# Kernel tuning notes

Hardware: AMD Instinct MI355X
Metric: run time of the kernel (lower is better)

## Reference

```python
import jax, jax.numpy as jnp
import numpy as np

EPS = 1e-5
HEADS = 2


def _batch_norm(x, gamma, beta, axes):
    # Training-mode batch norm (biased variance), channel axis = 1.
    m = jnp.mean(x, axes, keepdims=True)
    v = jnp.mean((x - m) ** 2, axes, keepdims=True)
    shape = [1] * x.ndim
    shape[1] = x.shape[1]
    return (x - m) * jax.lax.rsqrt(v + EPS) * gamma.reshape(shape) + beta.reshape(shape)


def setup_inputs() -> dict:
    key = jax.random.key(0)
    ks = jax.random.split(key, 6)
    b, n, H, W = 64, 2, 32, 32
    dim = H * W            # 1024
    inner = dim * HEADS    # 2048
    s = 0.02
    return {
        "x": jax.random.normal(ks[0], (b, n, H, W), jnp.float32),
        "Wq": jax.random.normal(ks[1], (inner, dim), jnp.float32) * s,
        "Wk": jax.random.normal(ks[2], (inner, dim), jnp.float32) * s,
        "Wv": jax.random.normal(ks[3], (inner, dim), jnp.float32) * s,
        "Wo": jax.random.normal(ks[4], (dim, inner), jnp.float32) * s,
        "bo": jnp.zeros((dim,), jnp.float32),
        "g_q": jnp.ones((2,), jnp.float32), "b_q": jnp.zeros((2,), jnp.float32),
        "g_k": jnp.ones((2,), jnp.float32), "b_k": jnp.zeros((2,), jnp.float32),
        "g_v": jnp.ones((2,), jnp.float32), "b_v": jnp.zeros((2,), jnp.float32),
        "g_bn": jnp.ones((2,), jnp.float32), "b_bn": jnp.zeros((2,), jnp.float32),
    }


def reference(x, Wq, Wk, Wv, Wo, bo, g_q, b_q, g_k, b_k, g_v, b_v, g_bn, b_bn):
    b, n, H, W = x.shape
    h = HEADS
    dim = H * W
    xf = x.reshape(b, n, dim)

    # to_q/to_k/to_v: Linear (no bias) + BatchNorm1d over channel dim n=2
    q = _batch_norm(xf @ Wq.T, g_q, b_q, (0, 2))  # (b, n, h*dim)
    k = _batch_norm(xf @ Wk.T, g_k, b_k, (0, 2))
    v = _batch_norm(xf @ Wv.T, g_v, b_v, (0, 2))

    def split_heads(t):  # b n (h d) -> b h n d
        return t.reshape(b, n, h, dim).transpose(0, 2, 1, 3)

    q, k, v = split_heads(q), split_heads(k), split_heads(v)

    # linear (kernelized) attention
    k_cumsum = k.sum(axis=-2)                                   # (b, h, d)
    D_inv = 1.0 / jnp.einsum('bhnd,bhd->bhn', q, k_cumsum)      # (b, h, n)
    context = jnp.einsum('bhnd,bhne->bhde', k, v)               # (b, h, d, d)
    out = jnp.einsum('bhde,bhnd,bhn->bhne', context, q, D_inv)  # (b, h, n, d)

    out = out.transpose(0, 2, 1, 3).reshape(b, n, h * dim)      # b h n d -> b n (h d)
    out = out @ Wo.T + bo                                       # to_out
    out = out.reshape(b, n, H, W)                               # dropout p=0 is identity
    return _batch_norm(out, g_bn, b_bn, (0, 2, 3))              # BatchNorm2d(2)
```

## Files before the change

kernel.cpp:

```cpp
#include <hip/hip_runtime.h>
#include <stdint.h>

typedef __bf16 bf16x8 __attribute__((ext_vector_type(8)));
typedef float f32x4 __attribute__((ext_vector_type(4)));

#define EPS 1e-5f

#define OFF_SQ    0
#define OFF_Q     4096
#define OFF_AHI   (OFF_Q + 3145728)
#define OFF_SO    (OFF_AHI + 524288)
#define OFF_PROJ  (OFF_SO + 4096)

static __device__ __forceinline__ unsigned short f2b(float f) {
  return __builtin_bit_cast(unsigned short, (__bf16)f);
}

__device__ __forceinline__ float wave_red(float v) {
#pragma unroll
  for (int o = 32; o > 0; o >>= 1) v += __shfl_down(v, o);
  return v;
}

#define GLDS16(g, l)                                             \
  __builtin_amdgcn_global_load_lds(                              \
      (const __attribute__((address_space(1))) void*)(g),        \
      (__attribute__((address_space(3))) void*)(l), 16, 0, 0)

static __device__ __forceinline__ void frag_split(const float* base, int p0,
                                                  bf16x8& hi, bf16x8& lo) {
  float4 v0 = *(const float4*)(base + p0 * 4);
  float4 v1 = *(const float4*)(base + p0 * 4 + 4);
  float a[8] = {v0.x, v0.y, v0.z, v0.w, v1.x, v1.y, v1.z, v1.w};
#pragma unroll
  for (int i = 0; i < 8; ++i) {
    __bf16 h = (__bf16)a[i];
    hi[i] = h;
    lo[i] = (__bf16)(a[i] - (float)h);
  }
}
static __device__ __forceinline__ bf16x8 frag_cvt(const float* base, int p0) {
  float4 v0 = *(const float4*)(base + p0 * 4);
  float4 v1 = *(const float4*)(base + p0 * 4 + 4);
  bf16x8 r;
  r[0] = (__bf16)v0.x; r[1] = (__bf16)v0.y; r[2] = (__bf16)v0.z; r[3] = (__bf16)v0.w;
  r[4] = (__bf16)v1.x; r[5] = (__bf16)v1.y; r[6] = (__bf16)v1.z; r[7] = (__bf16)v1.w;
  return r;
}

__global__ __launch_bounds__(256) void qkv_gemm(const float* __restrict__ x,
                                                const float* __restrict__ Wq,
                                                const float* __restrict__ Wk,
                                                const float* __restrict__ Wv,
                                                float* __restrict__ qkv,
                                                float* __restrict__ sq) {
  __shared__ alignas(16) float Af[3][128 * 64];
  __shared__ alignas(16) float Bf[3][32 * 64];
  __shared__ float red[16];

  int mat = blockIdx.x >> 6;
  int nt  = blockIdx.x & 63;
  const float* W = (mat == 0) ? Wq : ((mat == 1) ? Wk : Wv);
  float* outp = qkv + mat * 262144;

  int tid = threadIdx.x, w = tid >> 6, lane = tid & 63;
  int rsel = lane >> 4, ch = lane & 15;

#define STAGE_Q(c, tt) do {                                                      \
    _Pragma("unroll")                                                            \
    for (int j = 0; j < 8; ++j) {                                                \
      int rl = w * 32 + j * 4 + rsel;                                            \
      GLDS16(x + rl * 1024 + (tt) * 64 + ((ch ^ ((rl & 7) << 1)) << 2),          \
             &Af[c][(w * 32 + j * 4) * 64]);                                     \
    }                                                                            \
    _Pragma("unroll")                                                            \
    for (int j = 0; j < 2; ++j) {                                                \
      int rl = w * 8 + j * 4 + rsel;                                             \
      GLDS16(W + (nt * 32 + rl) * 1024 + (tt) * 64 +                             \
                 ((ch ^ ((rl & 7) << 1)) << 2),                                  \
             &Bf[c][(w * 8 + j * 4) * 64]);                                      \
    }                                                                            \
  } while (0)

  f32x4 acc[2][2];
#pragma unroll
  for (int m = 0; m < 2; ++m)
#pragma unroll
    for (int n = 0; n < 2; ++n) acc[m][n] = (f32x4){0.f, 0.f, 0.f, 0.f};

  STAGE_Q(0, 0);
  STAGE_Q(1, 1);
  __syncthreads();

#pragma unroll
  for (int t = 0; t < 16; ++t) {
    const int c = t % 3;
    bf16x8 fah[2][2], fal[2][2], fbh[2][2], fbl[2][2];
#pragma unroll
    for (int ks = 0; ks < 2; ++ks) {
      int kc = ks * 4 + rsel;
#pragma unroll
      for (int m = 0; m < 2; ++m) {
        int ra = w * 32 + m * 16 + (lane & 15);
        int p0 = (kc * 2) ^ ((ra & 7) << 1);
        frag_split(&Af[c][ra * 64], p0, fah[ks][m], fal[ks][m]);
      }
#pragma unroll
      for (int n = 0; n < 2; ++n) {
        int rb = n * 16 + (lane & 15);
        int p0 = (kc * 2) ^ ((rb & 7) << 1);
        frag_split(&Bf[c][rb * 64], p0, fbh[ks][n], fbl[ks][n]);
      }
    }
    if (t < 14) { STAGE_Q((t + 2) % 3, t + 2); }
#pragma unroll
    for (int ks = 0; ks < 2; ++ks)
#pragma unroll
      for (int m = 0; m < 2; ++m)
#pragma unroll
        for (int n = 0; n < 2; ++n) {
          acc[m][n] = __builtin_amdgcn_mfma_f32_16x16x32_bf16(fah[ks][m], fbh[ks][n], acc[m][n], 0, 0, 0);
          acc[m][n] = __builtin_amdgcn_mfma_f32_16x16x32_bf16(fah[ks][m], fbl[ks][n], acc[m][n], 0, 0, 0);
          acc[m][n] = __builtin_amdgcn_mfma_f32_16x16x32_bf16(fal[ks][m], fbh[ks][n], acc[m][n], 0, 0, 0);
        }
    if (t < 15) {
      if (t < 14) { asm volatile("s_waitcnt vmcnt(10) lgkmcnt(0)" ::: "memory"); }
      else        { asm volatile("s_waitcnt vmcnt(0) lgkmcnt(0)" ::: "memory"); }
      __builtin_amdgcn_sched_barrier(0);
      __builtin_amdgcn_s_barrier();
      __builtin_amdgcn_sched_barrier(0);
    }
  }
#undef STAGE_Q

  float s0 = 0, q0 = 0, s1 = 0, q1 = 0;
#pragma unroll
  for (int m = 0; m < 2; ++m)
#pragma unroll
    for (int n = 0; n < 2; ++n)
#pragma unroll
      for (int r = 0; r < 4; ++r) {
        int row = w * 32 + m * 16 + (lane >> 4) * 4 + r;
        int col = nt * 32 + n * 16 + (lane & 15);
        float v = acc[m][n][r];
        outp[row * 2048 + col] = v;
        if (r & 1) { s1 += v; q1 += v * v; } else { s0 += v; q0 += v * v; }
      }
  s0 = wave_red(s0); q0 = wave_red(q0); s1 = wave_red(s1); q1 = wave_red(q1);
  if (lane == 0) { red[w * 4 + 0] = s0; red[w * 4 + 1] = q0; red[w * 4 + 2] = s1; red[w * 4 + 3] = q1; }
  __syncthreads();
  if (tid == 0) {
    float a0 = 0, a1 = 0, a2 = 0, a3 = 0;
    for (int i = 0; i < 4; ++i) { a0 += red[i * 4 + 0]; a1 += red[i * 4 + 1]; a2 += red[i * 4 + 2]; a3 += red[i * 4 + 3]; }
    *(float4*)(sq + blockIdx.x * 4) = (float4){a0, a1, a2, a3};
  }
}

__global__ __launch_bounds__(256) void attn_kernel(const float* __restrict__ qkv,
                                                   const float* __restrict__ sq,
                                                   ushort* __restrict__ ahi,
                                                   const float* __restrict__ g_q, const float* __restrict__ b_q,
                                                   const float* __restrict__ g_k, const float* __restrict__ b_k,
                                                   const float* __restrict__ g_v, const float* __restrict__ b_v) {
  __shared__ float sm[12];
  __shared__ float red[16];
  __shared__ float bc[4];
  int bh = blockIdx.x, b = bh >> 1, h = bh & 1;
  int tid = threadIdx.x, w = tid >> 6, lane = tid & 63;

  if (tid < 192) {
    float4 p = *(const float4*)(sq + tid * 4);
    float a0 = wave_red(p.x), a1 = wave_red(p.y), a2 = wave_red(p.z), a3 = wave_red(p.w);
    if (lane == 0) { sm[w * 4 + 0] = a0; sm[w * 4 + 1] = a1; sm[w * 4 + 2] = a2; sm[w * 4 + 3] = a3; }
  }
  __syncthreads();

  const float cnt = 131072.f;
  float qs[2], qo[2], kc_[2], ko[2], vs[2], vo[2];
#pragma unroll
  for (int c = 0; c < 2; ++c) {
    float m, var, inv;
    m = sm[0 + 2 * c] / cnt; var = sm[1 + 2 * c] / cnt - m * m; inv = rsqrtf(var + EPS);
    qs[c] = g_q[c] * inv; qo[c] = b_q[c] - m * qs[c];
    m = sm[4 + 2 * c] / cnt; var = sm[5 + 2 * c] / cnt - m * m; inv = rsqrtf(var + EPS);
    kc_[c] = g_k[c] * inv; ko[c] = b_k[c] - m * kc_[c];
    m = sm[8 + 2 * c] / cnt; var = sm[9 + 2 * c] / cnt - m * m; inv = rsqrtf(var + EPS);
    vs[c] = g_v[c] * inv; vo[c] = b_v[c] - m * vs[c];
  }

  const float* Q = qkv;
  const float* K = qkv + 262144;
  const float* V = qkv + 524288;
  const float* q0p = Q + (b * 2 + 0) * 2048 + h * 1024;
  const float* q1p = Q + (b * 2 + 1) * 2048 + h * 1024;
  const float* k0p = K + (b * 2 + 0) * 2048 + h * 1024;
  const float* k1p = K + (b * 2 + 1) * 2048 + h * 1024;
  const float* v0p = V + (b * 2 + 0) * 2048 + h * 1024;
  const float* v1p = V + (b * 2 + 1) * 2048 + h * 1024;

  float p00 = 0, p01 = 0, p10 = 0, p11 = 0;
#pragma unroll
  for (int i = 0; i < 4; ++i) {
    int d = tid + i * 256;
    float a0 = q0p[d] * qs[0] + qo[0];
    float a1 = q1p[d] * qs[1] + qo[1];
    float c0 = k0p[d] * kc_[0] + ko[0];
    float c1 = k1p[d] * kc_[1] + ko[1];
    p00 += a0 * c0; p01 += a0 * c1; p10 += a1 * c0; p11 += a1 * c1;
  }
  p00 = wave_red(p00); p01 = wave_red(p01); p10 = wave_red(p10); p11 = wave_red(p11);
  if (lane == 0) { red[w * 4 + 0] = p00; red[w * 4 + 1] = p01; red[w * 4 + 2] = p10; red[w * 4 + 3] = p11; }
  __syncthreads();
  if (tid < 4) bc[tid] = red[0 + tid] + red[4 + tid] + red[8 + tid] + red[12 + tid];
  __syncthreads();
  float s00 = bc[0], s01 = bc[1], s10 = bc[2], s11 = bc[3];
  float di0 = 1.f / (s00 + s01), di1 = 1.f / (s10 + s11);
  int o0 = (b * 2 + 0) * 2048 + h * 1024;
  int o1 = (b * 2 + 1) * 2048 + h * 1024;
#pragma unroll
  for (int i = 0; i < 4; ++i) {
    int d = tid + i * 256;
    float v0 = v0p[d] * vs[0] + vo[0];
    float v1 = v1p[d] * vs[1] + vo[1];
    ahi[o0 + d] = f2b((s00 * v0 + s01 * v1) * di0);
    ahi[o1 + d] = f2b((s10 * v0 + s11 * v1) * di1);
  }
}

__global__ __launch_bounds__(256) void out_gemm(const ushort* __restrict__ ahi,
                                                const float* __restrict__ Wo,
                                                const float* __restrict__ bo,
                                                float* __restrict__ proj,
                                                float* __restrict__ so) {
  __shared__ alignas(16) ushort Ab[3][64 * 128];
  __shared__ alignas(16) float  Bf[3][16 * 128];
  __shared__ float red[16];

  int mt = blockIdx.x >> 6;
  int nt = blockIdx.x & 63;

  int tid = threadIdx.x, w = tid >> 6, lane = tid & 63;
  int rsel4 = lane >> 4, ch16 = lane & 15;
  int rsel2 = lane >> 5, ch32 = lane & 31;

#define STAGE_O(c, tt) do {                                                      \
    _Pragma("unroll")                                                            \
    for (int j = 0; j < 4; ++j) {                                                \
      int rl = w * 16 + j * 4 + rsel4;                                           \
      GLDS16(ahi + (mt * 64 + rl) * 2048 + (tt) * 128 +                          \
                 ((ch16 ^ (rl & 7)) << 3),                                       \
             &Ab[c][(w * 16 + j * 4) * 128]);                                    \
    }                                                                            \
    _Pragma("unroll")                                                            \
    for (int j = 0; j < 2; ++j) {                                                \
      int rl = w * 4 + j * 2 + rsel2;                                            \
      GLDS16(Wo + (nt * 16 + rl) * 2048 + (tt) * 128 +                           \
                 ((ch32 ^ ((rl & 7) << 1)) << 2),                                \
             &Bf[c][(w * 4 + j * 2) * 128]);                                     \
    }                                                                            \
  } while (0)

  f32x4 acc = (f32x4){0.f, 0.f, 0.f, 0.f};

  STAGE_O(0, 0);
  STAGE_O(1, 1);
  __syncthreads();

#pragma unroll
  for (int t = 0; t < 16; ++t) {
    const int c = t % 3;
    bf16x8 fa[4], fb[4];
#pragma unroll
    for (int ks = 0; ks < 4; ++ks) {
      int kc = ks * 4 + rsel4;
      int ra = w * 16 + (lane & 15);
      fa[ks] = *(const bf16x8*)(&Ab[c][ra * 128 + ((kc ^ (ra & 7)) << 3)]);
      int rb = lane & 15;
      int p0 = (kc * 2) ^ ((rb & 7) << 1);
      fb[ks] = frag_cvt(&Bf[c][rb * 128], p0);
    }
    if (t < 14) { STAGE_O((t + 2) % 3, t + 2); }
#pragma unroll
    for (int ks = 0; ks < 4; ++ks)
      acc = __builtin_amdgcn_mfma_f32_16x16x32_bf16(fa[ks], fb[ks], acc, 0, 0, 0);
    if (t < 15) {
      if (t < 14) { asm volatile("s_waitcnt vmcnt(6) lgkmcnt(0)" ::: "memory"); }
      else        { asm volatile("s_waitcnt vmcnt(0) lgkmcnt(0)" ::: "memory"); }
      __builtin_amdgcn_sched_barrier(0);
      __builtin_amdgcn_s_barrier();
      __builtin_amdgcn_sched_barrier(0);
    }
  }
#undef STAGE_O

  int col = nt * 16 + (lane & 15);
  float bov = bo[col];
  float s0 = 0, q0 = 0, s1 = 0, q1 = 0;
#pragma unroll
  for (int r = 0; r < 4; ++r) {
    int grow = mt * 64 + w * 16 + (lane >> 4) * 4 + r;
    float v = acc[r] + bov;
    proj[grow * 1024 + col] = v;
    if (r & 1) { s1 += v; q1 += v * v; } else { s0 += v; q0 += v * v; }
  }
  s0 = wave_red(s0); q0 = wave_red(q0); s1 = wave_red(s1); q1 = wave_red(q1);
  if (lane == 0) { red[w * 4 + 0] = s0; red[w * 4 + 1] = q0; red[w * 4 + 2] = s1; red[w * 4 + 3] = q1; }
  __syncthreads();
  if (tid == 0) {
    float a0 = 0, a1 = 0, a2 = 0, a3 = 0;
    for (int i = 0; i < 4; ++i) { a0 += red[i * 4 + 0]; a1 += red[i * 4 + 1]; a2 += red[i * 4 + 2]; a3 += red[i * 4 + 3]; }
    *(float4*)(so + blockIdx.x * 4) = (float4){a0, a1, a2, a3};
  }
}

__global__ __launch_bounds__(256) void final_kernel(const float* __restrict__ proj,
                                                    const float* __restrict__ so,
                                                    const float* __restrict__ g_bn,
                                                    const float* __restrict__ b_bn,
                                                    float* __restrict__ out) {
  __shared__ float sm[8];
  int tid = threadIdx.x, w = tid >> 6;
  int r = blockIdx.x;
  if (tid < 128) {
    float4 p = *(const float4*)(so + tid * 4);
    float a0 = wave_red(p.x), a1 = wave_red(p.y), a2 = wave_red(p.z), a3 = wave_red(p.w);
    if ((tid & 63) == 0) { sm[w * 4 + 0] = a0; sm[w * 4 + 1] = a1; sm[w * 4 + 2] = a2; sm[w * 4 + 3] = a3; }
  }
  __syncthreads();
  float s0 = sm[0] + sm[4], q0 = sm[1] + sm[5];
  float s1 = sm[2] + sm[6], q1 = sm[3] + sm[7];
  int ch = r & 1;
  float m = (ch ? s1 : s0) / 65536.f;
  float var = (ch ? q1 : q0) / 65536.f - m * m;
  float sc = g_bn[ch] * rsqrtf(var + EPS);
  float sh = b_bn[ch] - m * sc;
  float4 v = *(const float4*)(proj + r * 1024 + tid * 4);
  float4 o = {v.x * sc + sh, v.y * sc + sh, v.z * sc + sh, v.w * sc + sh};
  *(float4*)(out + r * 1024 + tid * 4) = o;
}

extern "C" void kernel_launch(void* const* d_in, const int* in_sizes, int n_in,
                              void* d_out, int out_size, void* d_ws, size_t ws_size,
                              hipStream_t stream) {
  (void)in_sizes; (void)n_in; (void)out_size; (void)ws_size;
  const float* x    = (const float*)d_in[0];
  const float* Wq   = (const float*)d_in[1];
  const float* Wk   = (const float*)d_in[2];
  const float* Wv   = (const float*)d_in[3];
  const float* Wo   = (const float*)d_in[4];
  const float* bo   = (const float*)d_in[5];
  const float* g_q  = (const float*)d_in[6];
  const float* b_q  = (const float*)d_in[7];
  const float* g_k  = (const float*)d_in[8];
  const float* b_k  = (const float*)d_in[9];
  const float* g_v  = (const float*)d_in[10];
  const float* b_v  = (const float*)d_in[11];
  const float* g_bn = (const float*)d_in[12];
  const float* b_bn = (const float*)d_in[13];
  char* ws = (char*)d_ws;
  float* out = (float*)d_out;

  float*  sq   = (float*)(ws + OFF_SQ);
  float*  qkv  = (float*)(ws + OFF_Q);
  ushort* ahi  = (ushort*)(ws + OFF_AHI);
  float*  so   = (float*)(ws + OFF_SO);
  float*  proj = (float*)(ws + OFF_PROJ);

  hipLaunchKernelGGL(qkv_gemm,     dim3(192), dim3(256), 0, stream, x, Wq, Wk, Wv, qkv, sq);
  hipLaunchKernelGGL(attn_kernel,  dim3(128), dim3(256), 0, stream, qkv, sq, ahi,
                     g_q, b_q, g_k, b_k, g_v, b_v);
  hipLaunchKernelGGL(out_gemm,     dim3(128), dim3(256), 0, stream, ahi, Wo, bo, proj, so);
  hipLaunchKernelGGL(final_kernel, dim3(128), dim3(256), 0, stream, proj, so, g_bn, b_bn, out);
}
```

Measured before the change: 45.73 us.

## Fuse attention into QKV and output GEMMs via algebraic dot-product partial sums

The QKV GEMM now computes Q, K and V in a single block per column tile, sharing the x tile across all three. Instead of writing Q and K to memory, it emits per-batch partial dot products and sums that the output GEMM combines with the batch-norm stats to rebuild the attention coefficients. The separate attention kernel is removed, and the normalized V mix is applied on the fly while building the A fragments of the output GEMM. This cuts one launch and most of the intermediate traffic. In exchange the grid shrinks to 64 larger blocks, and the output kernel runs a longer K loop over fp32 V.

```diff
diff --git a/kernel.cpp b/kernel.cpp
--- a/kernel.cpp
+++ b/kernel.cpp
@@ -6,15 +6,11 @@
 
 #define EPS 1e-5f
 
-#define OFF_SQ    0
-#define OFF_Q     4096
-#define OFF_AHI   (OFF_Q + 3145728)
-#define OFF_SO    (OFF_AHI + 524288)
+#define OFF_V     0
+#define OFF_SQ    1048576
+#define OFF_SDOT  (OFF_SQ + 4096)
+#define OFF_SO    (OFF_SDOT + 131072)
 #define OFF_PROJ  (OFF_SO + 4096)
-
-static __device__ __forceinline__ unsigned short f2b(float f) {
-  return __builtin_bit_cast(unsigned short, (__bf16)f);
-}
 
 __device__ __forceinline__ float wave_red(float v) {
 #pragma unroll
@@ -48,268 +44,319 @@
   return r;
 }
 
-__global__ __launch_bounds__(256) void qkv_gemm(const float* __restrict__ x,
+__global__ __launch_bounds__(512) void qkv_gemm(const float* __restrict__ x,
                                                 const float* __restrict__ Wq,
                                                 const float* __restrict__ Wk,
                                                 const float* __restrict__ Wv,
-                                                float* __restrict__ qkv,
-                                                float* __restrict__ sq) {
-  __shared__ alignas(16) float Af[3][128 * 64];
-  __shared__ alignas(16) float Bf[3][32 * 64];
-  __shared__ float red[16];
-
-  int mat = blockIdx.x >> 6;
-  int nt  = blockIdx.x & 63;
-  const float* W = (mat == 0) ? Wq : ((mat == 1) ? Wk : Wv);
-  float* outp = qkv + mat * 262144;
-
-  int tid = threadIdx.x, w = tid >> 6, lane = tid & 63;
-  int rsel = lane >> 4, ch = lane & 15;
-
-#define STAGE_Q(c, tt) do {                                                      \
-    _Pragma("unroll")                                                            \
-    for (int j = 0; j < 8; ++j) {                                                \
-      int rl = w * 32 + j * 4 + rsel;                                            \
-      GLDS16(x + rl * 1024 + (tt) * 64 + ((ch ^ ((rl & 7) << 1)) << 2),          \
-             &Af[c][(w * 32 + j * 4) * 64]);                                     \
-    }                                                                            \
-    _Pragma("unroll")                                                            \
-    for (int j = 0; j < 2; ++j) {                                                \
-      int rl = w * 8 + j * 4 + rsel;                                             \
-      GLDS16(W + (nt * 32 + rl) * 1024 + (tt) * 64 +                             \
-                 ((ch ^ ((rl & 7) << 1)) << 2),                                  \
-             &Bf[c][(w * 8 + j * 4) * 64]);                                      \
-    }                                                                            \
+                                                float* __restrict__ V,
+                                                float* __restrict__ sq,
+                                                float* __restrict__ sdot) {
+  __shared__ alignas(16) float Af[2][128 * 64];
+  __shared__ alignas(16) float Bf[3][96 * 64];
+  __shared__ float red[96];
+
+  const int nt = blockIdx.x;
+  const int tid = threadIdx.x, w = tid >> 6, lane = tid & 63;
+  const int rsel = lane >> 4, ch = lane & 15, l15 = lane & 15;
+
+#define STAGE_A(c, tt) do {                                                   \
+    _Pragma("unroll")                                                         \
+    for (int j = 0; j < 4; ++j) {                                             \
+      int rl = w * 16 + j * 4 + rsel;                                         \
+      GLDS16(x + rl * 1024 + (tt) * 64 + ((ch ^ ((rl & 7) << 1)) << 2),       \
+             &Af[c][(w * 16 + j * 4) * 64]);                                  \
+    }                                                                         \
   } while (0)
 
-  f32x4 acc[2][2];
-#pragma unroll
-  for (int m = 0; m < 2; ++m)
-#pragma unroll
-    for (int n = 0; n < 2; ++n) acc[m][n] = (f32x4){0.f, 0.f, 0.f, 0.f};
-
-  STAGE_Q(0, 0);
-  STAGE_Q(1, 1);
-  __syncthreads();
-
+#define STAGE_B(c, tt) do {                                                   \
+    _Pragma("unroll")                                                         \
+    for (int j = 0; j < 3; ++j) {                                             \
+      int br = w * 12 + j * 4;                                                \
+      int rl = br + rsel;                                                     \
+      const float* wb = (br < 32) ? Wq : ((br < 64) ? Wk : Wv);               \
+      GLDS16(wb + (nt * 32 + (rl & 31)) * 1024 + (tt) * 64 +                  \
+                 ((ch ^ ((rl & 7) << 1)) << 2),                               \
+             &Bf[c][br * 64]);                                                \
+    }                                                                         \
+  } while (0)
+
+  f32x4 aq[2], ak[2], av[2];
+#pragma unroll
+  for (int n = 0; n < 2; ++n) {
+    aq[n] = (f32x4){0.f, 0.f, 0.f, 0.f};
+    ak[n] = (f32x4){0.f, 0.f, 0.f, 0.f};
+    av[n] = (f32x4){0.f, 0.f, 0.f, 0.f};
+  }
+
+  STAGE_A(0, 0);
+  STAGE_B(0, 0);
+  STAGE_B(1, 1);
+  asm volatile("s_waitcnt vmcnt(3) lgkmcnt(0)" ::: "memory");
+  __builtin_amdgcn_sched_barrier(0);
+  __builtin_amdgcn_s_barrier();
+  __builtin_amdgcn_sched_barrier(0);
+
+  const int ra = w * 16 + l15;
 #pragma unroll
   for (int t = 0; t < 16; ++t) {
-    const int c = t % 3;
-    bf16x8 fah[2][2], fal[2][2], fbh[2][2], fbl[2][2];
+    const int cA = t & 1, cB = t % 3;
+    bf16x8 xh[2], xl[2];
+    bf16x8 qh[2][2], ql[2][2], kh[2][2], kl[2][2], vv[2][2];
 #pragma unroll
     for (int ks = 0; ks < 2; ++ks) {
-      int kc = ks * 4 + rsel;
-#pragma unroll
-      for (int m = 0; m < 2; ++m) {
-        int ra = w * 32 + m * 16 + (lane & 15);
-        int p0 = (kc * 2) ^ ((ra & 7) << 1);
-        frag_split(&Af[c][ra * 64], p0, fah[ks][m], fal[ks][m]);
+      const int kc = 2 * (ks * 4 + rsel);
+      frag_split(&Af[cA][ra * 64], kc ^ ((ra & 7) << 1), xh[ks], xl[ks]);
+#pragma unroll
+      for (int n = 0; n < 2; ++n) {
+        int rq = n * 16 + l15;
+        frag_split(&Bf[cB][rq * 64], kc ^ ((rq & 7) << 1), qh[ks][n], ql[ks][n]);
+        int rk = 32 + n * 16 + l15;
+        frag_split(&Bf[cB][rk * 64], kc ^ ((rk & 7) << 1), kh[ks][n], kl[ks][n]);
+        int rv = 64 + n * 16 + l15;
+        vv[ks][n] = frag_cvt(&Bf[cB][rv * 64], kc ^ ((rv & 7) << 1));
       }
+    }
+    if (t < 15) STAGE_A((t + 1) & 1, t + 1);
+    if (t < 14) STAGE_B((t + 2) % 3, t + 2);
+#pragma unroll
+    for (int ks = 0; ks < 2; ++ks)
 #pragma unroll
       for (int n = 0; n < 2; ++n) {
-        int rb = n * 16 + (lane & 15);
-        int p0 = (kc * 2) ^ ((rb & 7) << 1);
-        frag_split(&Bf[c][rb * 64], p0, fbh[ks][n], fbl[ks][n]);
+        aq[n] = __builtin_amdgcn_mfma_f32_16x16x32_bf16(xh[ks], qh[ks][n], aq[n], 0, 0, 0);
+        aq[n] = __builtin_amdgcn_mfma_f32_16x16x32_bf16(xh[ks], ql[ks][n], aq[n], 0, 0, 0);
+        aq[n] = __builtin_amdgcn_mfma_f32_16x16x32_bf16(xl[ks], qh[ks][n], aq[n], 0, 0, 0);
+        ak[n] = __builtin_amdgcn_mfma_f32_16x16x32_bf16(xh[ks], kh[ks][n], ak[n], 0, 0, 0);
+        ak[n] = __builtin_amdgcn_mfma_f32_16x16x32_bf16(xh[ks], kl[ks][n], ak[n], 0, 0, 0);
+        ak[n] = __builtin_amdgcn_mfma_f32_16x16x32_bf16(xl[ks], kh[ks][n], ak[n], 0, 0, 0);
+        av[n] = __builtin_amdgcn_mfma_f32_16x16x32_bf16(xh[ks], vv[ks][n], av[n], 0, 0, 0);
       }
-    }
-    if (t < 14) { STAGE_Q((t + 2) % 3, t + 2); }
-#pragma unroll
-    for (int ks = 0; ks < 2; ++ks)
-#pragma unroll
-      for (int m = 0; m < 2; ++m)
-#pragma unroll
-        for (int n = 0; n < 2; ++n) {
-          acc[m][n] = __builtin_amdgcn_mfma_f32_16x16x32_bf16(fah[ks][m], fbh[ks][n], acc[m][n], 0, 0, 0);
-          acc[m][n] = __builtin_amdgcn_mfma_f32_16x16x32_bf16(fah[ks][m], fbl[ks][n], acc[m][n], 0, 0, 0);
-          acc[m][n] = __builtin_amdgcn_mfma_f32_16x16x32_bf16(fal[ks][m], fbh[ks][n], acc[m][n], 0, 0, 0);
-        }
     if (t < 15) {
-      if (t < 14) { asm volatile("s_waitcnt vmcnt(10) lgkmcnt(0)" ::: "memory"); }
+      if (t < 14) { asm volatile("s_waitcnt vmcnt(3) lgkmcnt(0)" ::: "memory"); }
       else        { asm volatile("s_waitcnt vmcnt(0) lgkmcnt(0)" ::: "memory"); }
       __builtin_amdgcn_sched_barrier(0);
       __builtin_amdgcn_s_barrier();
       __builtin_amdgcn_sched_barrier(0);
     }
   }
-#undef STAGE_Q
-
+#undef STAGE_A
+#undef STAGE_B
+
+  float st[12];
+#pragma unroll
+  for (int j = 0; j < 12; ++j) st[j] = 0.f;
+#pragma unroll
+  for (int n = 0; n < 2; ++n)
+#pragma unroll
+    for (int r = 0; r < 4; ++r) {
+      int row = w * 16 + rsel * 4 + r;
+      int col = nt * 32 + n * 16 + l15;
+      float vq = aq[n][r], vk = ak[n][r], vvv = av[n][r];
+      V[row * 2048 + col] = vvv;
+      int p = (r & 1) * 2;
+      st[0 + p] += vq;  st[1 + p] += vq * vq;
+      st[4 + p] += vk;  st[5 + p] += vk * vk;
+      st[8 + p] += vvv; st[9 + p] += vvv * vvv;
+    }
+#pragma unroll
+  for (int j = 0; j < 12; ++j) st[j] = wave_red(st[j]);
+  if (lane == 0) {
+#pragma unroll
+    for (int j = 0; j < 12; ++j) red[w * 12 + j] = st[j];
+  }
+
+  float d8[2][8];
+#pragma unroll
+  for (int bb = 0; bb < 2; ++bb) {
+    int rb = bb * 2;
+    d8[bb][0] = aq[0][rb] * ak[0][rb]     + aq[1][rb] * ak[1][rb];
+    d8[bb][1] = aq[0][rb] * ak[0][rb + 1] + aq[1][rb] * ak[1][rb + 1];
+    d8[bb][2] = aq[0][rb + 1] * ak[0][rb]     + aq[1][rb + 1] * ak[1][rb];
+    d8[bb][3] = aq[0][rb + 1] * ak[0][rb + 1] + aq[1][rb + 1] * ak[1][rb + 1];
+    d8[bb][4] = aq[0][rb] + aq[1][rb];
+    d8[bb][5] = aq[0][rb + 1] + aq[1][rb + 1];
+    d8[bb][6] = ak[0][rb] + ak[1][rb];
+    d8[bb][7] = ak[0][rb + 1] + ak[1][rb + 1];
+  }
+#pragma unroll
+  for (int bb = 0; bb < 2; ++bb)
+#pragma unroll
+    for (int j = 0; j < 8; ++j) {
+      float v = d8[bb][j];
+      v += __shfl_xor(v, 1); v += __shfl_xor(v, 2);
+      v += __shfl_xor(v, 4); v += __shfl_xor(v, 8);
+      d8[bb][j] = v;
+    }
+  if (l15 == 0) {
+#pragma unroll
+    for (int bb = 0; bb < 2; ++bb) {
+      int b = w * 8 + rsel * 2 + bb;
+#pragma unroll
+      for (int j = 0; j < 8; ++j) sdot[(nt * 64 + b) * 8 + j] = d8[bb][j];
+    }
+  }
+  __syncthreads();
+  if (tid < 12) {
+    float s = 0.f;
+    for (int i = 0; i < 8; ++i) s += red[i * 12 + tid];
+    sq[tid * 64 + nt] = s;
+  }
+}
+
+__global__ __launch_bounds__(512) void out_fused(const float* __restrict__ V,
+                                                 const float* __restrict__ sq,
+                                                 const float* __restrict__ sdot,
+                                                 const float* __restrict__ Wo,
+                                                 const float* __restrict__ bo,
+                                                 const float* __restrict__ g_q, const float* __restrict__ b_q,
+                                                 const float* __restrict__ g_k, const float* __restrict__ b_k,
+                                                 const float* __restrict__ g_v, const float* __restrict__ b_v,
+                                                 float* __restrict__ proj,
+                                                 float* __restrict__ so) {
+  __shared__ alignas(16) float Af[3][128 * 64];
+  __shared__ alignas(16) float Bf[3][16 * 64];
+  __shared__ float Fl[1024];
+  __shared__ float sstat[12];
+  __shared__ float red[32];
+
+  const int nt = blockIdx.x;
+  const int tid = threadIdx.x, w = tid >> 6, lane = tid & 63;
+  const int rsel = lane >> 4, ch = lane & 15, l15 = lane & 15;
+
+#define STAGE_V(c, tt) do {                                                   \
+    _Pragma("unroll")                                                         \
+    for (int j = 0; j < 4; ++j) {                                             \
+      int rl = w * 16 + j * 4 + rsel;                                         \
+      GLDS16(V + rl * 2048 + (tt) * 64 + ((ch ^ ((rl & 7) << 1)) << 2),       \
+             &Af[c][(w * 16 + j * 4) * 64]);                                  \
+    }                                                                         \
+  } while (0)
+
+#define STAGE_W(c, tt) do {                                                   \
+    if (w < 4) {                                                              \
+      int rl = w * 4 + rsel;                                                  \
+      GLDS16(Wo + (nt * 16 + rl) * 2048 + (tt) * 64 +                         \
+                 ((ch ^ ((rl & 7) << 1)) << 2),                               \
+             &Bf[c][(w * 4) * 64]);                                           \
+    }                                                                         \
+  } while (0)
+
+  STAGE_V(0, 0); STAGE_W(0, 0);
+  STAGE_V(1, 1); STAGE_W(1, 1);
+
+  {
+    float s = sq[w * 64 + lane];
+    s = wave_red(s);
+    if (lane == 0) sstat[w] = s;
+    if (w < 4) {
+      float s2 = sq[(8 + w) * 64 + lane];
+      s2 = wave_red(s2);
+      if (lane == 0) sstat[8 + w] = s2;
+    }
+  }
+#pragma unroll
+  for (int e2 = 0; e2 < 2; ++e2) {
+    int e = tid * 2 + e2;
+    int b = e >> 4, hh = (e >> 3) & 1, j = e & 7;
+    float f = 0.f;
+    for (int i = 0; i < 32; ++i) f += sdot[((hh * 32 + i) * 64 + b) * 8 + j];
+    Fl[e] = f;
+  }
+  __syncthreads();
+
+  const int arow = w * 16 + l15, bidx = arow >> 1, nch = arow & 1;
+  float ca0, cb0, cg0, ca1, cb1, cg1;
+  {
+    const float CNT = 131072.f, CNTD = 1024.f;
+    float qm = sstat[0 + 2 * nch] / CNT, qv = sstat[1 + 2 * nch] / CNT - qm * qm;
+    float qs = g_q[nch] * rsqrtf(qv + EPS), qo = b_q[nch] - qm * qs;
+    float km0 = sstat[4] / CNT, kv0 = sstat[5] / CNT - km0 * km0;
+    float ks0 = g_k[0] * rsqrtf(kv0 + EPS), ko0 = b_k[0] - km0 * ks0;
+    float km1 = sstat[6] / CNT, kv1 = sstat[7] / CNT - km1 * km1;
+    float ks1 = g_k[1] * rsqrtf(kv1 + EPS), ko1 = b_k[1] - km1 * ks1;
+    float vm0 = sstat[8] / CNT, vv0 = sstat[9] / CNT - vm0 * vm0;
+    float vs0 = g_v[0] * rsqrtf(vv0 + EPS), vo0 = b_v[0] - vm0 * vs0;
+    float vm1 = sstat[10] / CNT, vv1 = sstat[11] / CNT - vm1 * vm1;
+    float vs1 = g_v[1] * rsqrtf(vv1 + EPS), vo1 = b_v[1] - vm1 * vs1;
+#pragma unroll
+    for (int h = 0; h < 2; ++h) {
+      const float* F = &Fl[bidx * 16 + h * 8];
+      float p0 = qs * ks0 * F[nch * 2 + 0] + qs * ko0 * F[4 + nch] +
+                 qo * ks0 * F[6] + qo * ko0 * CNTD;
+      float p1 = qs * ks1 * F[nch * 2 + 1] + qs * ko1 * F[4 + nch] +
+                 qo * ks1 * F[7] + qo * ko1 * CNTD;
+      float di = 1.f / (p0 + p1);
+      float a = di * p0 * vs0, bct = di * p1 * vs1;
+      float g = di * (p0 * vo0 + p1 * vo1);
+      if (h == 0) { ca0 = a; cb0 = bct; cg0 = g; }
+      else        { ca1 = a; cb1 = bct; cg1 = g; }
+    }
+  }
+
+  f32x4 acc = (f32x4){0.f, 0.f, 0.f, 0.f};
+  const int re = arow & ~1, ro = re + 1;
+
+#pragma unroll
+  for (int t = 0; t < 32; ++t) {
+    const int cc = t % 3;
+    const float mal = (t < 16) ? ca0 : ca1;
+    const float mbe = (t < 16) ? cb0 : cb1;
+    const float mga = (t < 16) ? cg0 : cg1;
+    bf16x8 fa[2], fb[2];
+#pragma unroll
+    for (int ks = 0; ks < 2; ++ks) {
+      const int kc = 2 * (ks * 4 + rsel);
+      const int pe = kc ^ ((re & 7) << 1), po = kc ^ ((ro & 7) << 1);
+      const float* bev = &Af[cc][re * 64];
+      const float* bov_ = &Af[cc][ro * 64];
+      float4 e0 = *(const float4*)(bev + pe * 4);
+      float4 e1 = *(const float4*)(bev + pe * 4 + 4);
+      float4 o0 = *(const float4*)(bov_ + po * 4);
+      float4 o1 = *(const float4*)(bov_ + po * 4 + 4);
+      float ve[8] = {e0.x, e0.y, e0.z, e0.w, e1.x, e1.y, e1.z, e1.w};
+      float vo[8] = {o0.x, o0.y, o0.z, o0.w, o1.x, o1.y, o1.z, o1.w};
+      bf16x8 r;
+#pragma unroll
+      for (int i = 0; i < 8; ++i)
+        r[i] = (__bf16)fmaf(mal, ve[i], fmaf(mbe, vo[i], mga));
+      fa[ks] = r;
+      fb[ks] = frag_cvt(&Bf[cc][l15 * 64], kc ^ ((l15 & 7) << 1));
+    }
+    if (t < 30) { STAGE_V((t + 2) % 3, t + 2); STAGE_W((t + 2) % 3, t + 2); }
+    acc = __builtin_amdgcn_mfma_f32_16x16x32_bf16(fa[0], fb[0], acc, 0, 0, 0);
+    acc = __builtin_amdgcn_mfma_f32_16x16x32_bf16(fa[1], fb[1], acc, 0, 0, 0);
+    if (t < 31) {
+      if (t < 30) {
+        if (w < 4) { asm volatile("s_waitcnt vmcnt(5) lgkmcnt(0)" ::: "memory"); }
+        else       { asm volatile("s_waitcnt vmcnt(4) lgkmcnt(0)" ::: "memory"); }
+      } else       { asm volatile("s_waitcnt vmcnt(0) lgkmcnt(0)" ::: "memory"); }
+      __builtin_amdgcn_sched_barrier(0);
+      __builtin_amdgcn_s_barrier();
+      __builtin_amdgcn_sched_barrier(0);
+    }
+  }
+#undef STAGE_V
+#undef STAGE_W
+
+  int col = nt * 16 + l15;
+  float bov = bo[col];
   float s0 = 0, q0 = 0, s1 = 0, q1 = 0;
 #pragma unroll
-  for (int m = 0; m < 2; ++m)
-#pragma unroll
-    for (int n = 0; n < 2; ++n)
-#pragma unroll
-      for (int r = 0; r < 4; ++r) {
-        int row = w * 32 + m * 16 + (lane >> 4) * 4 + r;
-        int col = nt * 32 + n * 16 + (lane & 15);
-        float v = acc[m][n][r];
-        outp[row * 2048 + col] = v;
-        if (r & 1) { s1 += v; q1 += v * v; } else { s0 += v; q0 += v * v; }
-      }
+  for (int r = 0; r < 4; ++r) {
+    int grow = w * 16 + rsel * 4 + r;
+    float v = acc[r] + bov;
+    proj[grow * 1024 + col] = v;
+    if (r & 1) { s1 += v; q1 += v * v; } else { s0 += v; q0 += v * v; }
+  }
   s0 = wave_red(s0); q0 = wave_red(q0); s1 = wave_red(s1); q1 = wave_red(q1);
   if (lane == 0) { red[w * 4 + 0] = s0; red[w * 4 + 1] = q0; red[w * 4 + 2] = s1; red[w * 4 + 3] = q1; }
   __syncthreads();
   if (tid == 0) {
     float a0 = 0, a1 = 0, a2 = 0, a3 = 0;
-    for (int i = 0; i < 4; ++i) { a0 += red[i * 4 + 0]; a1 += red[i * 4 + 1]; a2 += red[i * 4 + 2]; a3 += red[i * 4 + 3]; }
-    *(float4*)(sq + blockIdx.x * 4) = (float4){a0, a1, a2, a3};
-  }
-}
-
-__global__ __launch_bounds__(256) void attn_kernel(const float* __restrict__ qkv,
-                                                   const float* __restrict__ sq,
-                                                   ushort* __restrict__ ahi,
-                                                   const float* __restrict__ g_q, const float* __restrict__ b_q,
-                                                   const float* __restrict__ g_k, const float* __restrict__ b_k,
-                                                   const float* __restrict__ g_v, const float* __restrict__ b_v) {
-  __shared__ float sm[12];
-  __shared__ float red[16];
-  __shared__ float bc[4];
-  int bh = blockIdx.x, b = bh >> 1, h = bh & 1;
-  int tid = threadIdx.x, w = tid >> 6, lane = tid & 63;
-
-  if (tid < 192) {
-    float4 p = *(const float4*)(sq + tid * 4);
-    float a0 = wave_red(p.x), a1 = wave_red(p.y), a2 = wave_red(p.z), a3 = wave_red(p.w);
-    if (lane == 0) { sm[w * 4 + 0] = a0; sm[w * 4 + 1] = a1; sm[w * 4 + 2] = a2; sm[w * 4 + 3] = a3; }
-  }
-  __syncthreads();
-
-  const float cnt = 131072.f;
-  float qs[2], qo[2], kc_[2], ko[2], vs[2], vo[2];
-#pragma unroll
-  for (int c = 0; c < 2; ++c) {
-    float m, var, inv;
-    m = sm[0 + 2 * c] / cnt; var = sm[1 + 2 * c] / cnt - m * m; inv = rsqrtf(var + EPS);
-    qs[c] = g_q[c] * inv; qo[c] = b_q[c] - m * qs[c];
-    m = sm[4 + 2 * c] / cnt; var = sm[5 + 2 * c] / cnt - m * m; inv = rsqrtf(var + EPS);
-    kc_[c] = g_k[c] * inv; ko[c] = b_k[c] - m * kc_[c];
-    m = sm[8 + 2 * c] / cnt; var = sm[9 + 2 * c] / cnt - m * m; inv = rsqrtf(var + EPS);
-    vs[c] = g_v[c] * inv; vo[c] = b_v[c] - m * vs[c];
-  }
-
-  const float* Q = qkv;
-  const float* K = qkv + 262144;
-  const float* V = qkv + 524288;
-  const float* q0p = Q + (b * 2 + 0) * 2048 + h * 1024;
-  const float* q1p = Q + (b * 2 + 1) * 2048 + h * 1024;
-  const float* k0p = K + (b * 2 + 0) * 2048 + h * 1024;
-  const float* k1p = K + (b * 2 + 1) * 2048 + h * 1024;
-  const float* v0p = V + (b * 2 + 0) * 2048 + h * 1024;
-  const float* v1p = V + (b * 2 + 1) * 2048 + h * 1024;
-
-  float p00 = 0, p01 = 0, p10 = 0, p11 = 0;
-#pragma unroll
-  for (int i = 0; i < 4; ++i) {
-    int d = tid + i * 256;
-    float a0 = q0p[d] * qs[0] + qo[0];
-    float a1 = q1p[d] * qs[1] + qo[1];
-    float c0 = k0p[d] * kc_[0] + ko[0];
-    float c1 = k1p[d] * kc_[1] + ko[1];
-    p00 += a0 * c0; p01 += a0 * c1; p10 += a1 * c0; p11 += a1 * c1;
-  }
-  p00 = wave_red(p00); p01 = wave_red(p01); p10 = wave_red(p10); p11 = wave_red(p11);
-  if (lane == 0) { red[w * 4 + 0] = p00; red[w * 4 + 1] = p01; red[w * 4 + 2] = p10; red[w * 4 + 3] = p11; }
-  __syncthreads();
-  if (tid < 4) bc[tid] = red[0 + tid] + red[4 + tid] + red[8 + tid] + red[12 + tid];
-  __syncthreads();
-  float s00 = bc[0], s01 = bc[1], s10 = bc[2], s11 = bc[3];
-  float di0 = 1.f / (s00 + s01), di1 = 1.f / (s10 + s11);
-  int o0 = (b * 2 + 0) * 2048 + h * 1024;
-  int o1 = (b * 2 + 1) * 2048 + h * 1024;
-#pragma unroll
-  for (int i = 0; i < 4; ++i) {
-    int d = tid + i * 256;
-    float v0 = v0p[d] * vs[0] + vo[0];
-    float v1 = v1p[d] * vs[1] + vo[1];
-    ahi[o0 + d] = f2b((s00 * v0 + s01 * v1) * di0);
-    ahi[o1 + d] = f2b((s10 * v0 + s11 * v1) * di1);
-  }
-}
-
-__global__ __launch_bounds__(256) void out_gemm(const ushort* __restrict__ ahi,
-                                                const float* __restrict__ Wo,
-                                                const float* __restrict__ bo,
-                                                float* __restrict__ proj,
-                                                float* __restrict__ so) {
-  __shared__ alignas(16) ushort Ab[3][64 * 128];
-  __shared__ alignas(16) float  Bf[3][16 * 128];
-  __shared__ float red[16];
-
-  int mt = blockIdx.x >> 6;
-  int nt = blockIdx.x & 63;
-
-  int tid = threadIdx.x, w = tid >> 6, lane = tid & 63;
-  int rsel4 = lane >> 4, ch16 = lane & 15;
-  int rsel2 = lane >> 5, ch32 = lane & 31;
-
-#define STAGE_O(c, tt) do {                                                      \
-    _Pragma("unroll")                                                            \
-    for (int j = 0; j < 4; ++j) {                                                \
-      int rl = w * 16 + j * 4 + rsel4;                                           \
-      GLDS16(ahi + (mt * 64 + rl) * 2048 + (tt) * 128 +                          \
-                 ((ch16 ^ (rl & 7)) << 3),                                       \
-             &Ab[c][(w * 16 + j * 4) * 128]);                                    \
-    }                                                                            \
-    _Pragma("unroll")                                                            \
-    for (int j = 0; j < 2; ++j) {                                                \
-      int rl = w * 4 + j * 2 + rsel2;                                            \
-      GLDS16(Wo + (nt * 16 + rl) * 2048 + (tt) * 128 +                           \
-                 ((ch32 ^ ((rl & 7) << 1)) << 2),                                \
-             &Bf[c][(w * 4 + j * 2) * 128]);                                     \
-    }                                                                            \
-  } while (0)
-
-  f32x4 acc = (f32x4){0.f, 0.f, 0.f, 0.f};
-
-  STAGE_O(0, 0);
-  STAGE_O(1, 1);
-  __syncthreads();
-
-#pragma unroll
-  for (int t = 0; t < 16; ++t) {
-    const int c = t % 3;
-    bf16x8 fa[4], fb[4];
-#pragma unroll
-    for (int ks = 0; ks < 4; ++ks) {
-      int kc = ks * 4 + rsel4;
-      int ra = w * 16 + (lane & 15);
-      fa[ks] = *(const bf16x8*)(&Ab[c][ra * 128 + ((kc ^ (ra & 7)) << 3)]);
-      int rb = lane & 15;
-      int p0 = (kc * 2) ^ ((rb & 7) << 1);
-      fb[ks] = frag_cvt(&Bf[c][rb * 128], p0);
-    }
-    if (t < 14) { STAGE_O((t + 2) % 3, t + 2); }
-#pragma unroll
-    for (int ks = 0; ks < 4; ++ks)
-      acc = __builtin_amdgcn_mfma_f32_16x16x32_bf16(fa[ks], fb[ks], acc, 0, 0, 0);
-    if (t < 15) {
-      if (t < 14) { asm volatile("s_waitcnt vmcnt(6) lgkmcnt(0)" ::: "memory"); }
-      else        { asm volatile("s_waitcnt vmcnt(0) lgkmcnt(0)" ::: "memory"); }
-      __builtin_amdgcn_sched_barrier(0);
-      __builtin_amdgcn_s_barrier();
-      __builtin_amdgcn_sched_barrier(0);
-    }
-  }
-#undef STAGE_O
-
-  int col = nt * 16 + (lane & 15);
-  float bov = bo[col];
-  float s0 = 0, q0 = 0, s1 = 0, q1 = 0;
-#pragma unroll
-  for (int r = 0; r < 4; ++r) {
-    int grow = mt * 64 + w * 16 + (lane >> 4) * 4 + r;
-    float v = acc[r] + bov;
-    proj[grow * 1024 + col] = v;
-    if (r & 1) { s1 += v; q1 += v * v; } else { s0 += v; q0 += v * v; }
-  }
-  s0 = wave_red(s0); q0 = wave_red(q0); s1 = wave_red(s1); q1 = wave_red(q1);
-  if (lane == 0) { red[w * 4 + 0] = s0; red[w * 4 + 1] = q0; red[w * 4 + 2] = s1; red[w * 4 + 3] = q1; }
-  __syncthreads();
-  if (tid == 0) {
-    float a0 = 0, a1 = 0, a2 = 0, a3 = 0;
-    for (int i = 0; i < 4; ++i) { a0 += red[i * 4 + 0]; a1 += red[i * 4 + 1]; a2 += red[i * 4 + 2]; a3 += red[i * 4 + 3]; }
-    *(float4*)(so + blockIdx.x * 4) = (float4){a0, a1, a2, a3};
+    for (int i = 0; i < 8; ++i) {
+      a0 += red[i * 4 + 0]; a1 += red[i * 4 + 1];
+      a2 += red[i * 4 + 2]; a3 += red[i * 4 + 3];
+    }
+    *(float4*)(so + nt * 4) = (float4){a0, a1, a2, a3};
   }
 }
 
@@ -318,20 +365,18 @@
                                                     const float* __restrict__ g_bn,
                                                     const float* __restrict__ b_bn,
                                                     float* __restrict__ out) {
-  __shared__ float sm[8];
-  int tid = threadIdx.x, w = tid >> 6;
+  __shared__ float sm[4];
+  int tid = threadIdx.x;
   int r = blockIdx.x;
-  if (tid < 128) {
+  if (tid < 64) {
     float4 p = *(const float4*)(so + tid * 4);
     float a0 = wave_red(p.x), a1 = wave_red(p.y), a2 = wave_red(p.z), a3 = wave_red(p.w);
-    if ((tid & 63) == 0) { sm[w * 4 + 0] = a0; sm[w * 4 + 1] = a1; sm[w * 4 + 2] = a2; sm[w * 4 + 3] = a3; }
+    if (tid == 0) { sm[0] = a0; sm[1] = a1; sm[2] = a2; sm[3] = a3; }
   }
   __syncthreads();
-  float s0 = sm[0] + sm[4], q0 = sm[1] + sm[5];
-  float s1 = sm[2] + sm[6], q1 = sm[3] + sm[7];
   int ch = r & 1;
-  float m = (ch ? s1 : s0) / 65536.f;
-  float var = (ch ? q1 : q0) / 65536.f - m * m;
+  float m = (ch ? sm[2] : sm[0]) / 65536.f;
+  float var = (ch ? sm[3] : sm[1]) / 65536.f - m * m;
   float sc = g_bn[ch] * rsqrtf(var + EPS);
   float sh = b_bn[ch] - m * sc;
   float4 v = *(const float4*)(proj + r * 1024 + tid * 4);
@@ -360,15 +405,14 @@
   char* ws = (char*)d_ws;
   float* out = (float*)d_out;
 
-  float*  sq   = (float*)(ws + OFF_SQ);
-  float*  qkv  = (float*)(ws + OFF_Q);
-  ushort* ahi  = (ushort*)(ws + OFF_AHI);
-  float*  so   = (float*)(ws + OFF_SO);
-  float*  proj = (float*)(ws + OFF_PROJ);
-
-  hipLaunchKernelGGL(qkv_gemm,     dim3(192), dim3(256), 0, stream, x, Wq, Wk, Wv, qkv, sq);
-  hipLaunchKernelGGL(attn_kernel,  dim3(128), dim3(256), 0, stream, qkv, sq, ahi,
-                     g_q, b_q, g_k, b_k, g_v, b_v);
-  hipLaunchKernelGGL(out_gemm,     dim3(128), dim3(256), 0, stream, ahi, Wo, bo, proj, so);
+  float* V    = (float*)(ws + OFF_V);
+  float* sq   = (float*)(ws + OFF_SQ);
+  float* sdot = (float*)(ws + OFF_SDOT);
+  float* so   = (float*)(ws + OFF_SO);
+  float* proj = (float*)(ws + OFF_PROJ);
+
+  hipLaunchKernelGGL(qkv_gemm,     dim3(64),  dim3(512), 0, stream, x, Wq, Wk, Wv, V, sq, sdot);
+  hipLaunchKernelGGL(out_fused,    dim3(64),  dim3(512), 0, stream, V, sq, sdot, Wo, bo,
+                     g_q, b_q, g_k, b_k, g_v, b_v, proj, so);
   hipLaunchKernelGGL(final_kernel, dim3(128), dim3(256), 0, stream, proj, so, g_bn, b_bn, out);
 }
```

Result: slower. 86.75 us (+89.7%).
